# Kernel optimization log

Measured on AMD Instinct MI355X. Metric: run time of the kernel, lower is better.

## Reference

```python
import jax, jax.numpy as jnp
import numpy as np

D_IN = 768
D_OUT = 768
NUM_HEADS = 12
HEAD_DIM = D_OUT // NUM_HEADS


def setup_inputs() -> dict:
    key = jax.random.key(0)
    ks = jax.random.split(key, 9)
    s = 1.0 / np.sqrt(D_IN)
    x = jax.random.normal(ks[0], (8, 1024, D_IN), dtype=jnp.float32)
    Wq = jax.random.uniform(ks[1], (D_IN, D_OUT), jnp.float32, -s, s)
    Wk = jax.random.uniform(ks[2], (D_IN, D_OUT), jnp.float32, -s, s)
    Wv = jax.random.uniform(ks[3], (D_IN, D_OUT), jnp.float32, -s, s)
    Wo = jax.random.uniform(ks[4], (D_OUT, D_OUT), jnp.float32, -s, s)
    bq = jax.random.uniform(ks[5], (D_OUT,), jnp.float32, -s, s)
    bk = jax.random.uniform(ks[6], (D_OUT,), jnp.float32, -s, s)
    bv = jax.random.uniform(ks[7], (D_OUT,), jnp.float32, -s, s)
    bo = jax.random.uniform(ks[8], (D_OUT,), jnp.float32, -s, s)
    return {"x": x, "Wq": Wq, "bq": bq, "Wk": Wk, "bk": bk,
            "Wv": Wv, "bv": bv, "Wo": Wo, "bo": bo}


def reference(x, Wq, bq, Wk, bk, Wv, bv, Wo, bo):
    b, n, _ = x.shape
    # projections -> (b, heads, n, head_dim)
    def split_heads(t):
        return t.reshape(b, n, NUM_HEADS, HEAD_DIM).transpose(0, 2, 1, 3)
    q = split_heads(x @ Wq + bq)
    k = split_heads(x @ Wk + bk)
    v = split_heads(x @ Wv + bv)
    scale = 1.0 / jnp.sqrt(jnp.float32(HEAD_DIM)).astype(x.dtype)
    scores = jnp.einsum('bhqd,bhkd->bhqk', q, k) * scale
    attn = jax.nn.softmax(scores, axis=-1)  # dropout p=0.0 -> identity
    ctx = jnp.einsum('bhqk,bhkd->bhqd', attn, v)
    ctx = ctx.transpose(0, 2, 1, 3).reshape(b, n, D_OUT)
    return ctx @ Wo + bo
```

## Files before the change

kernel.cpp:

```cpp
#include <hip/hip_runtime.h>
#include <math.h>

#define D_MODEL 768
#define NHEAD  12
#define HDIM   64
#define SEQ    1024
#define BATCH  8
#define MTOT   (BATCH*SEQ)
#define QKV_LD 2304

typedef _Float16 f16;
typedef __attribute__((ext_vector_type(2))) __fp16 fp16x2;
typedef __attribute__((ext_vector_type(4))) _Float16 f16x4;
typedef __attribute__((ext_vector_type(8))) _Float16 f16x8;
typedef __attribute__((ext_vector_type(4))) float f32x4;
typedef __attribute__((ext_vector_type(16))) float f32x16;

union PFrag { unsigned u[4]; f16x8 v; };
union PackW { fp16x2 h; unsigned u; };

__device__ inline void gload_lds16(const void* g, void* l) {
    __builtin_amdgcn_global_load_lds(
        (const __attribute__((address_space(1))) void*)g,
        (__attribute__((address_space(3))) void*)l, 16, 0, 0);
}

__global__ __launch_bounds__(256) void cvt_f32_f16_fused(
    const float* __restrict__ in, f16* __restrict__ out, int n8,
    const float* __restrict__ bq, const float* __restrict__ bk,
    const float* __restrict__ bv, float* __restrict__ bqkv)
{
    const int i = blockIdx.x * 256 + threadIdx.x;
    if (i < n8) {
        const float4 a = *(const float4*)(in + (size_t)i * 8);
        const float4 b = *(const float4*)(in + (size_t)i * 8 + 4);
        f16x8 v;
        v[0] = (f16)a.x; v[1] = (f16)a.y; v[2] = (f16)a.z; v[3] = (f16)a.w;
        v[4] = (f16)b.x; v[5] = (f16)b.y; v[6] = (f16)b.z; v[7] = (f16)b.w;
        *(f16x8*)(out + (size_t)i * 8) = v;
    }
    if (i < QKV_LD)
        bqkv[i] = (i < 768) ? bq[i] : (i < 1536) ? bk[i - 768] : bv[i - 1536];
}

__global__ __launch_bounds__(256) void transpose_cvt_all(
    const float* __restrict__ Wq, const float* __restrict__ Wk,
    const float* __restrict__ Wv, const float* __restrict__ Wo,
    f16* __restrict__ Wqkv_t, f16* __restrict__ Wo_t)
{
    const int z = blockIdx.z;
    const float* src = (z == 0) ? Wq : (z == 1) ? Wk : (z == 2) ? Wv : Wo;
    f16* dst = (z < 3) ? (Wqkv_t + (size_t)z * 768 * 768) : Wo_t;

    __shared__ f16 tile[64][72];
    const int t  = threadIdx.x;
    const int k0 = blockIdx.y * 64;
    const int n0 = blockIdx.x * 64;
    {
        const int r  = t >> 4;
        const int c4 = (t & 15) * 4;
        #pragma unroll
        for (int u = 0; u < 4; ++u) {
            const int row = r + u * 16;
            const float4 a = *(const float4*)&src[(size_t)(k0 + row) * 768 + n0 + c4];
            tile[row][c4 + 0] = (f16)a.x;
            tile[row][c4 + 1] = (f16)a.y;
            tile[row][c4 + 2] = (f16)a.z;
            tile[row][c4 + 3] = (f16)a.w;
        }
    }
    __syncthreads();
    {
        const int rn = t >> 3;
        const int ck = (t & 7) * 8;
        #pragma unroll
        for (int u = 0; u < 2; ++u) {
            const int n = rn + u * 32;
            f16x8 v;
            #pragma unroll
            for (int q = 0; q < 8; ++q) v[q] = tile[ck + q][n];
            *(f16x8*)&dst[(size_t)(n0 + n) * 768 + k0 + ck] = v;
        }
    }
}

template<typename OUT_T>
__global__ __launch_bounds__(256) void gemm_f16_tn(
    const f16* __restrict__ A, const f16* __restrict__ Bt,
    const float* __restrict__ bias, OUT_T* __restrict__ C,
    int M, int N, int K, int nb)
{
    __shared__ f16 As[128 * 64];
    __shared__ f16 Bs[128 * 64];

    const int t    = threadIdx.x;
    const int l15  = (t & 63) & 15;
    const int lg   = (t & 63) >> 4;
    const int w    = t >> 6;
    const int wrow = (w >> 1) * 64;
    const int wcol = (w & 1) * 64;

    const int orig = blockIdx.x;
    const int cpx  = gridDim.x >> 3;
    const int nid  = (orig & 7) * cpx + (orig >> 3);
    const int row0 = (nid / nb) * 128;
    const int col0 = (nid % nb) * 128;

    int src_row[4], src_koff[4], lds_off[4];
    #pragma unroll
    for (int i = 0; i < 4; ++i) {
        const int c = t + 256 * i;
        const int r = c >> 3;
        src_row[i]  = r;
        src_koff[i] = ((((c & 7) - (r >> 1)) & 7)) * 8;
        lds_off[i]  = c * 16;
    }

    int a_off[4][2], b_off[4][2];
    #pragma unroll
    for (int i = 0; i < 4; ++i) {
        const int ra = wrow + i * 16 + l15;
        const int rb = wcol + i * 16 + l15;
        #pragma unroll
        for (int s = 0; s < 2; ++s) {
            a_off[i][s] = ra * 128 + (((s * 4 + lg + (ra >> 1)) & 7) * 16);
            b_off[i][s] = rb * 128 + (((s * 4 + lg + (rb >> 1)) & 7) * 16);
        }
    }

    f32x4 acc[4][4];
    #pragma unroll
    for (int i = 0; i < 4; ++i)
        #pragma unroll
        for (int j = 0; j < 4; ++j)
            acc[i][j] = (f32x4){0.f, 0.f, 0.f, 0.f};

    const f16* Abase = A  + (size_t)row0 * K;
    const f16* Bbase = Bt + (size_t)col0 * K;

    for (int k0 = 0; k0 < K; k0 += 64) {
        #pragma unroll
        for (int i = 0; i < 4; ++i) {
            gload_lds16(Abase + (size_t)src_row[i] * K + k0 + src_koff[i],
                        (char*)As + lds_off[i]);
            gload_lds16(Bbase + (size_t)src_row[i] * K + k0 + src_koff[i],
                        (char*)Bs + lds_off[i]);
        }
        __syncthreads();

        #pragma unroll
        for (int s = 0; s < 2; ++s) {
            f16x8 af[4], bf[4];
            #pragma unroll
            for (int i = 0; i < 4; ++i) {
                af[i] = *(const f16x8*)((const char*)As + a_off[i][s]);
                bf[i] = *(const f16x8*)((const char*)Bs + b_off[i][s]);
            }
            #pragma unroll
            for (int i = 0; i < 4; ++i)
                #pragma unroll
                for (int j = 0; j < 4; ++j)
                    acc[i][j] = __builtin_amdgcn_mfma_f32_16x16x32_f16(
                        af[i], bf[j], acc[i][j], 0, 0, 0);
        }
        __syncthreads();
    }

    #pragma unroll
    for (int j = 0; j < 4; ++j) {
        const int col = col0 + wcol + j * 16 + l15;
        const float bj = bias[col];
        #pragma unroll
        for (int i = 0; i < 4; ++i) {
            const int row = row0 + wrow + i * 16 + lg * 4;
            #pragma unroll
            for (int q = 0; q < 4; ++q)
                C[(size_t)(row + q) * N + col] = (OUT_T)(acc[i][j][q] + bj);
        }
    }
}

#define RESCALE_THR 10.0f
#define QMAP(r, hh) (((r) & 3) + 8 * ((r) >> 2) + 4 * (hh))

__global__ __launch_bounds__(256, 3) void attn_f16(
    const f16* __restrict__ QKV, f16* __restrict__ O)
{
    __shared__ f16 KsB[2][64 * 64];
    __shared__ f16 VtB[2][64 * 64];

    const int t   = threadIdx.x;
    const int w   = t >> 6;
    const int l   = t & 63;
    const int l31 = l & 31;
    const int h   = l >> 5;
    const int sl  = (l & 7) << 4;

    const int orig = blockIdx.x;
    const int s    = (orig & 7) * 96 + (orig >> 3);
    const int bh   = s >> 3;
    const int qb   = s & 7;
    const int b  = bh / NHEAD;
    const int hd = bh % NHEAD;
    const int q0 = qb * 128;

    const size_t rowbase = (size_t)b * SEQ;
    const int qcol = hd * HDIM;
    const int kcol = 768 + hd * HDIM;
    const int vcol = 1536 + hd * HDIM;

    const f16 hsc = (f16)(0.125f * 1.4426950408889634f);
    f16x8 qf[4];
    #pragma unroll
    for (int dc = 0; dc < 4; ++dc) {
        f16x8 v = *(const f16x8*)(QKV
            + (rowbase + q0 + w * 32 + l31) * QKV_LD
            + qcol + dc * 16 + h * 8);
        #pragma unroll
        for (int j = 0; j < 8; ++j) v[j] *= hsc;
        qf[dc] = v;
    }

    f32x16 ctx[2];
    #pragma unroll
    for (int dt = 0; dt < 2; ++dt)
        #pragma unroll
        for (int r = 0; r < 16; ++r) ctx[dt][r] = 0.f;
    float mrun = -INFINITY;
    float lrun = 0.f;

    const int cb  = w * 16;
    const int vk0 = (l & 15) * 4;
    const int vd0 = ((l >> 4) + 4 * w) * 4;
    const f16* kptr = QKV + (rowbase + l)   * QKV_LD + kcol + cb;
    const f16* vptr = QKV + (rowbase + vk0) * QKV_LD + vcol + vd0;
    const size_t step = (size_t)64 * QKV_LD;

    f16x8 kr0, kr1;
    f16x4 vr[4];
    kr0 = *(const f16x8*)(kptr);
    kr1 = *(const f16x8*)(kptr + 8);
    #pragma unroll
    for (int i = 0; i < 4; ++i)
        vr[i] = *(const f16x4*)(vptr + (size_t)i * QKV_LD);

    {
        char* Kd = (char*)KsB[0];
        char* Vd = (char*)VtB[0];
        *(f16x8*)(Kd + l * 128 + ((cb * 2)      ^ sl)) = kr0;
        *(f16x8*)(Kd + l * 128 + ((cb * 2 + 16) ^ sl)) = kr1;
        #pragma unroll
        for (int di = 0; di < 4; ++di) {
            f16x4 wt;
            #pragma unroll
            for (int i = 0; i < 4; ++i) wt[i] = vr[i][di];
            *(f16x4*)(Vd + (vd0 + di) * 128
                         + ((vk0 * 2) ^ (((vd0 + di) & 7) << 4))) = wt;
        }
    }
    kr0 = *(const f16x8*)(kptr + step);
    kr1 = *(const f16x8*)(kptr + step + 8);
    #pragma unroll
    for (int i = 0; i < 4; ++i)
        vr[i] = *(const f16x4*)(vptr + step + (size_t)i * QKV_LD);
    __syncthreads();

    for (int kt = 0; kt < SEQ / 64; ++kt) {
        const int p = kt & 1;
        const char* Kp = (const char*)KsB[p];
        const char* Vp = (const char*)VtB[p];

        f32x16 sacc[2];
        __builtin_amdgcn_s_setprio(1);
        #pragma unroll
        for (int kk = 0; kk < 2; ++kk) {
            f32x16 a;
            #pragma unroll
            for (int r = 0; r < 16; ++r) a[r] = 0.f;
            #pragma unroll
            for (int dc = 0; dc < 4; ++dc) {
                const f16x8 ka = *(const f16x8*)(Kp + (kk * 32 + l31) * 128
                                                    + ((dc * 32 + h * 16) ^ sl));
                a = __builtin_amdgcn_mfma_f32_32x32x16_f16(ka, qf[dc], a, 0, 0, 0);
            }
            sacc[kk] = a;
        }
        __builtin_amdgcn_s_setprio(0);

        {
            float tmax = sacc[0][0];
            #pragma unroll
            for (int r = 1; r < 16; ++r) tmax = fmaxf(tmax, sacc[0][r]);
            #pragma unroll
            for (int r = 0; r < 16; ++r) tmax = fmaxf(tmax, sacc[1][r]);
            tmax = fmaxf(tmax, __shfl_xor(tmax, 32));

            if (__any(tmax > mrun + RESCALE_THR)) {
                const float mnew = fmaxf(mrun, tmax);
                const float corr = exp2f(mrun - mnew);
                mrun = mnew;
                lrun *= corr;
                #pragma unroll
                for (int r = 0; r < 16; ++r) {
                    const float cr = __shfl(corr, QMAP(r, h));
                    ctx[0][r] *= cr;
                    ctx[1][r] *= cr;
                }
            }

            float ps = 0.f;
            #pragma unroll
            for (int kk = 0; kk < 2; ++kk)
                #pragma unroll
                for (int r = 0; r < 16; ++r) {
                    const float pe = exp2f(sacc[kk][r] - mrun);
                    ps += pe;
                    sacc[kk][r] = pe;
                }
            ps += __shfl_xor(ps, 32);
            lrun += ps;
        }

        unsigned paw[4][4];
        #pragma unroll
        for (int kk = 0; kk < 2; ++kk) {
            unsigned dw[8];
            #pragma unroll
            for (int i = 0; i < 8; ++i) {
                PackW u;
                u.h = __builtin_amdgcn_cvt_pkrtz(sacc[kk][2 * i], sacc[kk][2 * i + 1]);
                dw[i] = u.u;
            }
            const unsigned t0 = (unsigned)__shfl_xor((int)(h ? dw[0] : dw[2]), 32);
            const unsigned t1 = (unsigned)__shfl_xor((int)(h ? dw[1] : dw[3]), 32);
            const unsigned t2 = (unsigned)__shfl_xor((int)(h ? dw[4] : dw[6]), 32);
            const unsigned t3 = (unsigned)__shfl_xor((int)(h ? dw[5] : dw[7]), 32);
            paw[2 * kk][0]     = h ? t0    : dw[0];
            paw[2 * kk][1]     = h ? t1    : dw[1];
            paw[2 * kk][2]     = h ? dw[2] : t0;
            paw[2 * kk][3]     = h ? dw[3] : t1;
            paw[2 * kk + 1][0] = h ? t2    : dw[4];
            paw[2 * kk + 1][1] = h ? t3    : dw[5];
            paw[2 * kk + 1][2] = h ? dw[6] : t2;
            paw[2 * kk + 1][3] = h ? dw[7] : t3;
        }

        if (kt < SEQ / 64 - 1) {
            char* Kd = (char*)KsB[p ^ 1];
            char* Vd = (char*)VtB[p ^ 1];
            *(f16x8*)(Kd + l * 128 + ((cb * 2)      ^ sl)) = kr0;
            *(f16x8*)(Kd + l * 128 + ((cb * 2 + 16) ^ sl)) = kr1;
            #pragma unroll
            for (int di = 0; di < 4; ++di) {
                f16x4 wt;
                #pragma unroll
                for (int i = 0; i < 4; ++i) wt[i] = vr[i][di];
                *(f16x4*)(Vd + (vd0 + di) * 128
                             + ((vk0 * 2) ^ (((vd0 + di) & 7) << 4))) = wt;
            }
            if (kt < SEQ / 64 - 2) {
                const f16* kp = kptr + (size_t)(kt + 2) * step;
                const f16* vp = vptr + (size_t)(kt + 2) * step;
                kr0 = *(const f16x8*)(kp);
                kr1 = *(const f16x8*)(kp + 8);
                #pragma unroll
                for (int i = 0; i < 4; ++i)
                    vr[i] = *(const f16x4*)(vp + (size_t)i * QKV_LD);
            }
        }

        __builtin_amdgcn_s_setprio(1);
        #pragma unroll
        for (int c = 0; c < 4; ++c) {
            PFrag pf;
            pf.u[0] = paw[c][0]; pf.u[1] = paw[c][1];
            pf.u[2] = paw[c][2]; pf.u[3] = paw[c][3];
            #pragma unroll
            for (int dt = 0; dt < 2; ++dt) {
                const f16x8 vb = *(const f16x8*)(Vp + (dt * 32 + l31) * 128
                                                    + ((c * 32 + h * 16) ^ sl));
                ctx[dt] = __builtin_amdgcn_mfma_f32_32x32x16_f16(pf.v, vb, ctx[dt], 0, 0, 0);
            }
        }
        __builtin_amdgcn_s_setprio(0);

        __syncthreads();
    }

    {
        const float inv = 1.0f / lrun;
        #pragma unroll
        for (int r = 0; r < 16; ++r) {
            const float iv = __shfl(inv, QMAP(r, h));
            const size_t row = rowbase + q0 + w * 32 + QMAP(r, h);
            O[row * D_MODEL + qcol + l31]      = (f16)(ctx[0][r] * iv);
            O[row * D_MODEL + qcol + 32 + l31] = (f16)(ctx[1][r] * iv);
        }
    }
}

extern "C" void kernel_launch(void* const* d_in, const int* in_sizes, int n_in,
                              void* d_out, int out_size, void* d_ws, size_t ws_size,
                              hipStream_t stream) {
    const float* x  = (const float*)d_in[0];
    const float* Wq = (const float*)d_in[1];
    const float* bq = (const float*)d_in[2];
    const float* Wk = (const float*)d_in[3];
    const float* bk = (const float*)d_in[4];
    const float* Wv = (const float*)d_in[5];
    const float* bv = (const float*)d_in[6];
    const float* Wo = (const float*)d_in[7];
    const float* bo = (const float*)d_in[8];
    float* out = (float*)d_out;

    char* ws = (char*)d_ws;
    f16*   QKV     = (f16*)(ws);
    f16*   xh      = (f16*)(ws + 37748736);
    f16*   ctxh    = (f16*)(ws + 37748736 + 12582912);
    f16*   Wqkv_t  = (f16*)(ws + 37748736 + 2 * 12582912);
    f16*   Wo_t    = (f16*)(ws + 37748736 + 2 * 12582912 + 3538944);
    float* bqkv    = (float*)(ws + 37748736 + 2 * 12582912 + 3538944 + 1179648);

    hipLaunchKernelGGL(cvt_f32_f16_fused, dim3(MTOT * D_MODEL / 8 / 256), dim3(256), 0, stream,
                       x, xh, MTOT * D_MODEL / 8, bq, bk, bv, bqkv);
    hipLaunchKernelGGL(transpose_cvt_all, dim3(12, 12, 4), dim3(256), 0, stream,
                       Wq, Wk, Wv, Wo, Wqkv_t, Wo_t);

    hipLaunchKernelGGL((gemm_f16_tn<f16>), dim3((QKV_LD / 128) * (MTOT / 128)), dim3(256), 0, stream,
                       xh, Wqkv_t, bqkv, QKV, MTOT, QKV_LD, D_MODEL, QKV_LD / 128);

    hipLaunchKernelGGL(attn_f16, dim3((SEQ / 128) * BATCH * NHEAD), dim3(256), 0, stream,
                       QKV, ctxh);

    hipLaunchKernelGGL((gemm_f16_tn<float>), dim3((D_MODEL / 128) * (MTOT / 128)), dim3(256), 0, stream,
                       ctxh, Wo_t, bo, out, MTOT, D_MODEL, D_MODEL, D_MODEL / 128);
}
```

Baseline: 139.7 us.

## Software-pipeline attention loop by computing next tile's QK scores before PV

Restructures the flash-attention inner loop so that the QK^T MFMAs for tile kt+1 are issued right after the softmax of tile kt, before the PV product. K is now prefetched one stage deeper: tile kt+2 goes into shared memory and tile kt+3 into registers. A prologue computes the first score tile. The aim is to let the softmax VALU/shuffle work overlap with MFMA work and to hide LDS/global latency. In exchange, the score accumulators stay live for longer, which raises register pressure, and the control flow now has more edge cases at the loop ends.

Measured after the change: 142.6 us. +2.1%, slower.

```diff
diff --git a/kernel.cpp b/kernel.cpp
--- a/kernel.cpp
+++ b/kernel.cpp
@@ -238,12 +238,12 @@
 
     f16x8 kr0, kr1;
     f16x4 vr[4];
+
     kr0 = *(const f16x8*)(kptr);
     kr1 = *(const f16x8*)(kptr + 8);
     #pragma unroll
     for (int i = 0; i < 4; ++i)
         vr[i] = *(const f16x4*)(vptr + (size_t)i * QKV_LD);
-
     {
         char* Kd = (char*)KsB[0];
         char* Vd = (char*)VtB[0];
@@ -260,17 +260,21 @@
     }
     kr0 = *(const f16x8*)(kptr + step);
     kr1 = *(const f16x8*)(kptr + step + 8);
+    {
+        char* Kd = (char*)KsB[1];
+        *(f16x8*)(Kd + l * 128 + ((cb * 2)      ^ sl)) = kr0;
+        *(f16x8*)(Kd + l * 128 + ((cb * 2 + 16) ^ sl)) = kr1;
+    }
     #pragma unroll
     for (int i = 0; i < 4; ++i)
         vr[i] = *(const f16x4*)(vptr + step + (size_t)i * QKV_LD);
+    kr0 = *(const f16x8*)(kptr + 2 * step);
+    kr1 = *(const f16x8*)(kptr + 2 * step + 8);
     __syncthreads();
 
-    for (int kt = 0; kt < SEQ / 64; ++kt) {
-        const int p = kt & 1;
-        const char* Kp = (const char*)KsB[p];
-        const char* Vp = (const char*)VtB[p];
-
-        f32x16 sacc[2];
+    f32x16 sacc[2];
+    {
+        const char* Kp = (const char*)KsB[0];
         __builtin_amdgcn_s_setprio(1);
         #pragma unroll
         for (int kk = 0; kk < 2; ++kk) {
@@ -286,7 +290,10 @@
             sacc[kk] = a;
         }
         __builtin_amdgcn_s_setprio(0);
-
+    }
+    __syncthreads();
+
+    for (int kt = 0; kt < SEQ / 64; ++kt) {
         {
             float tmax = sacc[0][0];
             #pragma unroll
@@ -346,10 +353,31 @@
         }
 
         if (kt < SEQ / 64 - 1) {
-            char* Kd = (char*)KsB[p ^ 1];
-            char* Vd = (char*)VtB[p ^ 1];
+            const char* Kp = (const char*)KsB[(kt + 1) & 1];
+            __builtin_amdgcn_s_setprio(1);
+            #pragma unroll
+            for (int kk = 0; kk < 2; ++kk) {
+                f32x16 a;
+                #pragma unroll
+                for (int r = 0; r < 16; ++r) a[r] = 0.f;
+                #pragma unroll
+                for (int dc = 0; dc < 4; ++dc) {
+                    const f16x8 ka = *(const f16x8*)(Kp + (kk * 32 + l31) * 128
+                                                        + ((dc * 32 + h * 16) ^ sl));
+                    a = __builtin_amdgcn_mfma_f32_32x32x16_f16(ka, qf[dc], a, 0, 0, 0);
+                }
+                sacc[kk] = a;
+            }
+            __builtin_amdgcn_s_setprio(0);
+        }
+
+        if (kt < SEQ / 64 - 2) {
+            char* Kd = (char*)KsB[kt & 1];
             *(f16x8*)(Kd + l * 128 + ((cb * 2)      ^ sl)) = kr0;
             *(f16x8*)(Kd + l * 128 + ((cb * 2 + 16) ^ sl)) = kr1;
+        }
+        if (kt < SEQ / 64 - 1) {
+            char* Vd = (char*)VtB[(kt + 1) & 1];
             #pragma unroll
             for (int di = 0; di < 4; ++di) {
                 f16x4 wt;
@@ -358,33 +386,38 @@
                 *(f16x4*)(Vd + (vd0 + di) * 128
                              + ((vk0 * 2) ^ (((vd0 + di) & 7) << 4))) = wt;
             }
-            if (kt < SEQ / 64 - 2) {
-                const f16* kp = kptr + (size_t)(kt + 2) * step;
-                const f16* vp = vptr + (size_t)(kt + 2) * step;
-                kr0 = *(const f16x8*)(kp);
-                kr1 = *(const f16x8*)(kp + 8);
-                #pragma unroll
-                for (int i = 0; i < 4; ++i)
-                    vr[i] = *(const f16x4*)(vp + (size_t)i * QKV_LD);
-            }
-        }
-
-        __builtin_amdgcn_s_setprio(1);
-        #pragma unroll
-        for (int c = 0; c < 4; ++c) {
-            PFrag pf;
-            pf.u[0] = paw[c][0]; pf.u[1] = paw[c][1];
-            pf.u[2] = paw[c][2]; pf.u[3] = paw[c][3];
-            #pragma unroll
-            for (int dt = 0; dt < 2; ++dt) {
-                const f16x8 vb = *(const f16x8*)(Vp + (dt * 32 + l31) * 128
-                                                    + ((c * 32 + h * 16) ^ sl));
-                ctx[dt] = __builtin_amdgcn_mfma_f32_32x32x16_f16(pf.v, vb, ctx[dt], 0, 0, 0);
-            }
-        }
-        __builtin_amdgcn_s_setprio(0);
-
-        __syncthreads();
+        }
+        if (kt < SEQ / 64 - 3) {
+            const f16* kp = kptr + (size_t)(kt + 3) * step;
+            kr0 = *(const f16x8*)(kp);
+            kr1 = *(const f16x8*)(kp + 8);
+        }
+        if (kt < SEQ / 64 - 2) {
+            const f16* vp = vptr + (size_t)(kt + 2) * step;
+            #pragma unroll
+            for (int i = 0; i < 4; ++i)
+                vr[i] = *(const f16x4*)(vp + (size_t)i * QKV_LD);
+        }
+
+        {
+            const char* Vp = (const char*)VtB[kt & 1];
+            __builtin_amdgcn_s_setprio(1);
+            #pragma unroll
+            for (int c = 0; c < 4; ++c) {
+                PFrag pf;
+                pf.u[0] = paw[c][0]; pf.u[1] = paw[c][1];
+                pf.u[2] = paw[c][2]; pf.u[3] = paw[c][3];
+                #pragma unroll
+                for (int dt = 0; dt < 2; ++dt) {
+                    const f16x8 vb = *(const f16x8*)(Vp + (dt * 32 + l31) * 128
+                                                        + ((c * 32 + h * 16) ^ sl));
+                    ctx[dt] = __builtin_amdgcn_mfma_f32_32x32x16_f16(pf.v, vb, ctx[dt], 0, 0, 0);
+                }
+            }
+            __builtin_amdgcn_s_setprio(0);
+        }
+
+        if (kt < SEQ / 64 - 1) __syncthreads();
     }
 
     {
```
